# Kernel optimization log

Measured on AMD Instinct MI355X. Metric: run time of the kernel, lower is better.

The kernel has to match this reference:

```python
import jax, jax.numpy as jnp
import numpy as np
from jax import lax

# Dims: c1=256, num_heads = c1//64 = 4, head_dim=64, key_dim=32 (attn_ratio=0.5)
B, C, H, W = 4, 256, 64, 64
NH, HD, KD = 4, 64, 32
HQKV = C + 2 * NH * KD  # 512
RED = 16  # channel-attention reduction


def setup_inputs() -> dict:
    key = jax.random.key(0)
    ks = jax.random.split(key, 11)
    s = 0.02
    return {
        "x": jax.random.normal(ks[0], (B, C, H, W), jnp.float32),
        # Attention params (Conv = conv+BN folded into conv+bias)
        "w_qkv": jax.random.normal(ks[1], (HQKV, C), jnp.float32) * s,   # 1x1 conv
        "b_qkv": jax.random.normal(ks[2], (HQKV,), jnp.float32) * s,
        "w_proj": jax.random.normal(ks[3], (C, C), jnp.float32) * s,     # 1x1 conv
        "b_proj": jax.random.normal(ks[4], (C,), jnp.float32) * s,
        "w_pe": jax.random.normal(ks[5], (C, 1, 3, 3), jnp.float32) * s, # depthwise 3x3
        "b_pe": jax.random.normal(ks[6], (C,), jnp.float32) * s,
        # ChannelAttention params (1x1 convs, no bias)
        "w_fc1": jax.random.normal(ks[7], (C // RED, C), jnp.float32) * s,
        "w_fc2": jax.random.normal(ks[8], (C, C // RED), jnp.float32) * s,
        # SpatialAttention conv (2->1 channels, 3x3, no bias)
        "w_sa": jax.random.normal(ks[9], (1, 2, 3, 3), jnp.float32) * s,
    }


def _conv1x1(x, w, b=None):
    y = jnp.einsum('bchw,oc->bohw', x, w)
    if b is not None:
        y = y + b[None, :, None, None]
    return y


def _dwconv3(x, w, b):
    y = lax.conv_general_dilated(
        x, w, window_strides=(1, 1), padding='SAME',
        feature_group_count=x.shape[1],
        dimension_numbers=('NCHW', 'OIHW', 'NCHW'))
    return y + b[None, :, None, None]


def reference(x, w_qkv, b_qkv, w_proj, b_proj, w_pe, b_pe, w_fc1, w_fc2, w_sa):
    Bb, Cc, Hh, Ww = x.shape
    N = Hh * Ww
    scale = KD ** -0.5

    # --- Attention (asymmetric q/k/v head dims) ---
    qkv = _conv1x1(x, w_qkv, b_qkv).reshape(Bb, NH, 2 * KD + HD, N)
    q = qkv[:, :, :KD]            # [B,h,KD,N]
    k = qkv[:, :, KD:2 * KD]      # [B,h,KD,N]
    v = qkv[:, :, 2 * KD:]        # [B,h,HD,N]
    attn = jnp.einsum('bhkn,bhkm->bhnm', q, k) * scale  # [B,h,N,N]
    attn = jax.nn.softmax(attn, axis=-1)
    out = jnp.einsum('bhdm,bhnm->bhdn', v, attn).reshape(Bb, Cc, Hh, Ww)
    out = out + _dwconv3(v.reshape(Bb, Cc, Hh, Ww), w_pe, b_pe)
    out = _conv1x1(out, w_proj, b_proj)
    x = x + out

    # --- Channel attention (shared MLP on avg+max pooled features) ---
    def mlp(u):  # u: [B,C]
        return jnp.maximum(u @ w_fc1.T, 0.0) @ w_fc2.T
    avg = jnp.mean(x, axis=(2, 3))
    mx = jnp.max(x, axis=(2, 3))
    ca = jax.nn.sigmoid(mlp(avg) + mlp(mx))[:, :, None, None]
    x = x * ca

    # --- Spatial attention ---
    sa_in = jnp.stack([jnp.mean(x, axis=1), jnp.max(x, axis=1)], axis=1)  # [B,2,H,W]
    sa = lax.conv_general_dilated(
        sa_in, w_sa, window_strides=(1, 1), padding='SAME',
        dimension_numbers=('NCHW', 'OIHW', 'NCHW'))
    sa = jax.nn.sigmoid(sa)
    return x * sa
```

## Files before the change

### kernel.cpp

```cpp
#include <hip/hip_runtime.h>
#include <hip/hip_bf16.h>

typedef __bf16 bf16;
typedef __bf16 bf16x4 __attribute__((ext_vector_type(4)));
typedef __bf16 bf16x8 __attribute__((ext_vector_type(8)));
typedef float f32x4 __attribute__((ext_vector_type(4)));

#define B_ 4
#define C_ 256
#define NH_ 4
#define KD_ 32
#define HD_ 64
#define N_ 4096
#define HQKV_ 512

__global__ __launch_bounds__(256) void k_convw(const float* wq, const float* wp,
                                               bf16* wqb, bf16* wpb) {
    int i = blockIdx.x * 256 + threadIdx.x;
    if (i < HQKV_ * C_) wqb[i] = (bf16)wq[i];
    if (i < C_ * C_)    wpb[i] = (bf16)wp[i];
}

__global__ __launch_bounds__(256) void k_transpose(const float* __restrict__ x,
                                                   bf16* __restrict__ xT) {
    __shared__ float tile[64][65];
    int b = blockIdx.z, c0 = blockIdx.y * 64, n0 = blockIdx.x * 64;
    int t = threadIdx.x;
    int lane = t & 63, wv = t >> 6;
    for (int k = 0; k < 16; ++k) {
        int cl = k * 4 + wv;
        tile[cl][lane] = x[((size_t)(b * C_ + c0 + cl)) * N_ + n0 + lane];
    }
    __syncthreads();
    for (int k = 0; k < 16; ++k) {
        int nl = k * 4 + wv;
        xT[((size_t)(b * N_ + n0 + nl)) * C_ + c0 + lane] = (bf16)tile[lane][nl];
    }
}

__global__ __launch_bounds__(256) void k_qkv(const bf16* __restrict__ wqb,
                                             const bf16* __restrict__ xT,
                                             const float* __restrict__ bias,
                                             bf16* __restrict__ qt, bf16* __restrict__ kt,
                                             bf16* __restrict__ vb) {
    int n0 = blockIdx.x * 64, o0 = blockIdx.y * 64, b = blockIdx.z;
    int t = threadIdx.x, w = t >> 6, l = t & 63, lr = l & 15, lg = l >> 4;
    const bf16* arow = wqb + (size_t)(o0 + 16 * w + lr) * C_ + 8 * lg;
    const bf16* brow = xT + ((size_t)b * N_ + n0 + lr) * C_ + 8 * lg;
    f32x4 acc[4];
    f32x4 zz = {0.f, 0.f, 0.f, 0.f};
    acc[0] = zz; acc[1] = zz; acc[2] = zz; acc[3] = zz;
    for (int kk = 0; kk < C_; kk += 32) {
        bf16x8 a = *(const bf16x8*)(arow + kk);
#pragma unroll
        for (int tt = 0; tt < 4; ++tt) {
            bf16x8 bb = *(const bf16x8*)(brow + (size_t)tt * 16 * C_ + kk);
            acc[tt] = __builtin_amdgcn_mfma_f32_16x16x32_bf16(a, bb, acc[tt], 0, 0, 0);
        }
    }
    const float scale = 0.25506953076085663f;
#pragma unroll
    for (int tt = 0; tt < 4; ++tt) {
        int n = n0 + 16 * tt + lr;
#pragma unroll
        for (int j = 0; j < 4; ++j) {
            int o = o0 + 16 * w + 4 * lg + j;
            float val = acc[tt][j] + bias[o];
            int h = o >> 7, r = o & 127;
            size_t bh = (size_t)(b * NH_ + h);
            if (r < KD_)            qt[(bh * N_ + n) * KD_ + r] = (bf16)(val * scale);
            else if (r < 2 * KD_)   kt[(bh * N_ + n) * KD_ + (r - KD_)] = (bf16)val;
            else                    vb[(bh * HD_ + (r - 2 * KD_)) * N_ + n] = (bf16)val;
        }
    }
}

__global__ __launch_bounds__(256) void k_attn(const bf16* __restrict__ qt,
                                              const bf16* __restrict__ kt,
                                              const bf16* __restrict__ vb,
                                              float* __restrict__ attnT) {
    __shared__ bf16 ldsK[2][64 * KD_];
    __shared__ bf16 ldsV[2][64 * 64];
    __shared__ bf16 ldsP[4][32 * 72];
    int n0 = blockIdx.x * 128;
    int bh = blockIdx.y;
    int b = bh >> 2, h = bh & 3;
    int t = threadIdx.x, w = t >> 6, l = t & 63, lr = l & 15, lg = l >> 4;

    bf16x8 aq0 = *(const bf16x8*)(qt + ((size_t)bh * N_ + n0 + 32 * w + lr) * KD_ + 8 * lg);
    bf16x8 aq1 = *(const bf16x8*)(qt + ((size_t)bh * N_ + n0 + 32 * w + 16 + lr) * KD_ + 8 * lg);

    int krow = 16 * w + (l >> 2);
    const bf16* kg = kt + ((size_t)bh * N_ + krow) * KD_ + 8 * (l & 3);
    bf16* kwp = &ldsK[0][0] + krow * KD_ + 8 * ((l & 3) ^ (krow & 3));
    int vrow0 = 16 * w + (l >> 3);
    int vrow1 = vrow0 + 8;
    const bf16* vg0 = vb + ((size_t)bh * HD_ + vrow0) * N_ + 8 * (l & 7);
    const bf16* vg1 = vb + ((size_t)bh * HD_ + vrow1) * N_ + 8 * (l & 7);
    bf16* vwp0 = &ldsV[0][0] + vrow0 * 64 + 8 * ((l & 7) ^ (vrow0 & 7));
    bf16* vwp1 = &ldsV[0][0] + vrow1 * 64 + 8 * ((l & 7) ^ (vrow1 & 7));

    f32x4 zz = {0.f, 0.f, 0.f, 0.f};
    f32x4 Lacc0 = zz, Lacc1 = zz;
    f32x4 oacc[2][4];
#pragma unroll
    for (int q = 0; q < 2; ++q)
#pragma unroll
        for (int dt = 0; dt < 4; ++dt) oacc[q][dt] = zz;
    bf16* myp = &ldsP[w][0];

    bf16x8 rk = *(const bf16x8*)(kg);
    bf16x8 rv0 = *(const bf16x8*)(vg0);
    bf16x8 rv1 = *(const bf16x8*)(vg1);

    int cur = 0;
    for (int m0 = 0; m0 < N_; m0 += 64) {
        *(bf16x8*)(kwp + cur * (64 * KD_)) = rk;
        *(bf16x8*)(vwp0 + cur * (64 * 64)) = rv0;
        *(bf16x8*)(vwp1 + cur * (64 * 64)) = rv1;
        if (m0 + 64 < N_) {
            rk  = *(const bf16x8*)(kg + (size_t)(m0 + 64) * KD_);
            rv0 = *(const bf16x8*)(vg0 + m0 + 64);
            rv1 = *(const bf16x8*)(vg1 + m0 + 64);
        }
        __syncthreads();
        const bf16* kb_ = &ldsK[cur][0];
        const bf16* vb_ = &ldsV[cur][0];
        f32x4 s0[4], s1[4];
#pragma unroll
        for (int tt = 0; tt < 4; ++tt) {
            bf16x8 kf = *(const bf16x8*)(kb_ + (16 * tt + lr) * KD_ + 8 * (lg ^ (lr & 3)));
            s0[tt] = __builtin_amdgcn_mfma_f32_16x16x32_bf16(kf, aq0, zz, 0, 0, 0);
            s1[tt] = __builtin_amdgcn_mfma_f32_16x16x32_bf16(kf, aq1, zz, 0, 0, 0);
        }
#pragma unroll
        for (int tt = 0; tt < 4; ++tt) {
            bf16x4 p0, p1;
#pragma unroll
            for (int j = 0; j < 4; ++j) {
                float pv0 = __builtin_amdgcn_exp2f(s0[tt][j]);
                float pv1 = __builtin_amdgcn_exp2f(s1[tt][j]);
                Lacc0[j] += pv0; Lacc1[j] += pv1;
                p0[j] = (bf16)pv0; p1[j] = (bf16)pv1;
            }
            *(bf16x4*)(myp + lr * 72 + 16 * tt + 4 * lg) = p0;
            *(bf16x4*)(myp + (16 + lr) * 72 + 16 * tt + 4 * lg) = p1;
        }
#pragma unroll
        for (int ks = 0; ks < 2; ++ks) {
            bf16x8 pa0 = *(const bf16x8*)(myp + lr * 72 + 32 * ks + 8 * lg);
            bf16x8 pa1 = *(const bf16x8*)(myp + (16 + lr) * 72 + 32 * ks + 8 * lg);
#pragma unroll
            for (int dt = 0; dt < 4; ++dt) {
                bf16x8 vf = *(const bf16x8*)(vb_ + (16 * dt + lr) * 64 + 8 * ((4 * ks + lg) ^ (lr & 7)));
                oacc[0][dt] = __builtin_amdgcn_mfma_f32_16x16x32_bf16(pa0, vf, oacc[0][dt], 0, 0, 0);
                oacc[1][dt] = __builtin_amdgcn_mfma_f32_16x16x32_bf16(pa1, vf, oacc[1][dt], 0, 0, 0);
            }
        }
        cur ^= 1;
    }
    float Lp0 = Lacc0[0] + Lacc0[1] + Lacc0[2] + Lacc0[3];
    float Lp1 = Lacc1[0] + Lacc1[1] + Lacc1[2] + Lacc1[3];
    Lp0 += __shfl_xor(Lp0, 16); Lp0 += __shfl_xor(Lp0, 32);
    Lp1 += __shfl_xor(Lp1, 16); Lp1 += __shfl_xor(Lp1, 32);
    float inv0[4], inv1[4];
#pragma unroll
    for (int j = 0; j < 4; ++j) {
        inv0[j] = 1.f / __shfl(Lp0, 4 * lg + j);
        inv1[j] = 1.f / __shfl(Lp1, 4 * lg + j);
    }
#pragma unroll
    for (int dt = 0; dt < 4; ++dt)
#pragma unroll
        for (int j = 0; j < 4; ++j) {
            int n = n0 + 32 * w + 4 * lg + j;
            int d = h * HD_ + 16 * dt + lr;
            attnT[((size_t)b * N_ + n) * C_ + d] = oacc[0][dt][j] * inv0[j];
            attnT[((size_t)b * N_ + n + 16) * C_ + d] = oacc[1][dt][j] * inv1[j];
        }
}

__global__ __launch_bounds__(256) void k_pe_add(const float* __restrict__ attnT,
                                                const bf16* __restrict__ vb,
                                                const float* __restrict__ wpe,
                                                const float* __restrict__ bpe,
                                                bf16* __restrict__ yT) {
    __shared__ float vt[64 * 199];
    int hh = blockIdx.x, c0 = blockIdx.y * 64, b = blockIdx.z;
    int t = threadIdx.x, lane = t & 63, wg = t >> 6;

    if (t < 192) {
        int c_l = t >> 2, kh2 = t & 3;
        if (kh2 < 3) {
            vt[c_l * 199 + kh2 * 66 + 0] = 0.f;
            vt[c_l * 199 + kh2 * 66 + 65] = 0.f;
        }
    }
    if (t >= 192) {
        int u = t - 192;
        int c_l = 48 + (u >> 2), kh2 = u & 3;
        if (kh2 < 3) {
            vt[c_l * 199 + kh2 * 66 + 0] = 0.f;
            vt[c_l * 199 + kh2 * 66 + 65] = 0.f;
        }
    }
#pragma unroll
    for (int kh = 0; kh < 3; ++kh) {
        int hh2 = hh + kh - 1;
        bool ok = (hh2 >= 0 && hh2 < 64);
        for (int ci = 0; ci < 16; ++ci) {
            int c_l = wg * 16 + ci;
            float val = ok ? (float)vb[((size_t)(b * C_ + c0 + c_l)) * N_ + hh2 * 64 + lane] : 0.f;
            vt[c_l * 199 + kh * 66 + 1 + lane] = val;
        }
    }
    __syncthreads();

    int c = c0 + lane;
    float w9[9];
#pragma unroll
    for (int k = 0; k < 9; ++k) w9[k] = wpe[c * 9 + k];
    float bc = bpe[c];
    const float* vrow = vt + lane * 199;

#pragma unroll
    for (int wi = 0; wi < 16; ++wi) {
        int w = wg * 16 + wi;
        float acc = bc;
#pragma unroll
        for (int kh = 0; kh < 3; ++kh)
#pragma unroll
            for (int kw = 0; kw < 3; ++kw)
                acc += vrow[kh * 66 + w + kw] * w9[kh * 3 + kw];
        int n = hh * 64 + w;
        size_t idx = ((size_t)b * N_ + n) * C_ + c;
        yT[idx] = (bf16)(attnT[idx] + acc);
    }
}

__global__ __launch_bounds__(256) void k_proj(const bf16* __restrict__ wpb,
                                              const bf16* __restrict__ yT,
                                              const float* __restrict__ bias,
                                              const float* __restrict__ x,
                                              float* __restrict__ x2) {
    int n0 = blockIdx.x * 64, o0 = blockIdx.y * 64, b = blockIdx.z;
    int t = threadIdx.x, w = t >> 6, l = t & 63, lr = l & 15, lg = l >> 4;
    const bf16* arow = wpb + (size_t)(o0 + 16 * w + lr) * C_ + 8 * lg;
    const bf16* brow = yT + ((size_t)b * N_ + n0 + lr) * C_ + 8 * lg;
    f32x4 acc[4];
    f32x4 zz = {0.f, 0.f, 0.f, 0.f};
    acc[0] = zz; acc[1] = zz; acc[2] = zz; acc[3] = zz;
    for (int kk = 0; kk < C_; kk += 32) {
        bf16x8 a = *(const bf16x8*)(arow + kk);
#pragma unroll
        for (int tt = 0; tt < 4; ++tt) {
            bf16x8 bb = *(const bf16x8*)(brow + (size_t)tt * 16 * C_ + kk);
            acc[tt] = __builtin_amdgcn_mfma_f32_16x16x32_bf16(a, bb, acc[tt], 0, 0, 0);
        }
    }
#pragma unroll
    for (int tt = 0; tt < 4; ++tt) {
        int n = n0 + 16 * tt + lr;
#pragma unroll
        for (int j = 0; j < 4; ++j) {
            int o = o0 + 16 * w + 4 * lg + j;
            size_t idx = ((size_t)b * C_ + o) * N_ + n;
            x2[idx] = x[idx] + acc[tt][j] + bias[o];
        }
    }
}

__global__ __launch_bounds__(256) void k_ca_red(const float* __restrict__ x2,
                                                float* __restrict__ avg, float* __restrict__ mx) {
    int bc = blockIdx.x;
    int t = threadIdx.x;
    const float* row = x2 + (size_t)bc * N_;
    float s = 0.f, m = -1e30f;
    for (int i = t; i < N_; i += 256) { float v = row[i]; s += v; m = fmaxf(m, v); }
#pragma unroll
    for (int d = 1; d < 64; d <<= 1) { s += __shfl_xor(s, d); m = fmaxf(m, __shfl_xor(m, d)); }
    __shared__ float ss[4], sm[4];
    int w = t >> 6;
    if ((t & 63) == 0) { ss[w] = s; sm[w] = m; }
    __syncthreads();
    if (t == 0) {
        avg[bc] = (ss[0] + ss[1] + ss[2] + ss[3]) / (float)N_;
        mx[bc] = fmaxf(fmaxf(sm[0], sm[1]), fmaxf(sm[2], sm[3]));
    }
}

__global__ __launch_bounds__(256) void k_ca_mlp(const float* __restrict__ avg,
                                                const float* __restrict__ mx,
                                                const float* __restrict__ wfc1,
                                                const float* __restrict__ wfc2,
                                                float* __restrict__ ca) {
    int b = blockIdx.x, t = threadIdx.x;
    __shared__ float hsum[16];
    if (t < 16) {
        const float* w1 = wfc1 + t * C_;
        float ha = 0.f, hm = 0.f;
        for (int c = 0; c < C_; ++c) { ha += avg[b * C_ + c] * w1[c]; hm += mx[b * C_ + c] * w1[c]; }
        hsum[t] = fmaxf(ha, 0.f) + fmaxf(hm, 0.f);
    }
    __syncthreads();
    float o = 0.f;
    const float* w2 = wfc2 + t * 16;
#pragma unroll
    for (int r = 0; r < 16; ++r) o += hsum[r] * w2[r];
    ca[b * C_ + t] = 1.f / (1.f + __expf(-o));
}

__global__ __launch_bounds__(256) void k_sa_red(const float* __restrict__ x2,
                                                const float* __restrict__ ca,
                                                float* __restrict__ sain) {
    int b = blockIdx.y;
    int n = blockIdx.x * 256 + threadIdx.x;
    __shared__ float cal[C_];
    cal[threadIdx.x] = ca[b * C_ + threadIdx.x];
    __syncthreads();
    float s = 0.f, m = -1e30f;
    for (int c = 0; c < C_; ++c) {
        float v = x2[((size_t)b * C_ + c) * N_ + n] * cal[c];
        s += v; m = fmaxf(m, v);
    }
    sain[((size_t)b * 2 + 0) * N_ + n] = s * (1.f / C_);
    sain[((size_t)b * 2 + 1) * N_ + n] = m;
}

__global__ __launch_bounds__(256) void k_final(const float* __restrict__ x2,
                                               const float* __restrict__ ca,
                                               const float* __restrict__ sain,
                                               const float* __restrict__ wsa,
                                               float* __restrict__ out) {
    int b = blockIdx.y;
    int n = blockIdx.x * 256 + threadIdx.x;
    __shared__ float cal[C_];
    cal[threadIdx.x] = ca[b * C_ + threadIdx.x];
    __syncthreads();
    int hh = n >> 6, ww = n & 63;
    float acc = 0.f;
#pragma unroll
    for (int i = 0; i < 2; ++i)
#pragma unroll
        for (int kh = 0; kh < 3; ++kh) {
            int hh2 = hh + kh - 1;
            if (hh2 < 0 || hh2 >= 64) continue;
#pragma unroll
            for (int kw = 0; kw < 3; ++kw) {
                int ww2 = ww + kw - 1;
                if (ww2 < 0 || ww2 >= 64) continue;
                acc += sain[((size_t)b * 2 + i) * N_ + hh2 * 64 + ww2] * wsa[i * 9 + kh * 3 + kw];
            }
        }
    float sa = 1.f / (1.f + __expf(-acc));
    for (int c = 0; c < C_; ++c) {
        size_t idx = ((size_t)b * C_ + c) * N_ + n;
        out[idx] = x2[idx] * cal[c] * sa;
    }
}

extern "C" void kernel_launch(void* const* d_in, const int* in_sizes, int n_in,
                              void* d_out, int out_size, void* d_ws, size_t ws_size,
                              hipStream_t stream) {
    const float* x     = (const float*)d_in[0];
    const float* wqkv  = (const float*)d_in[1];
    const float* bqkv  = (const float*)d_in[2];
    const float* wproj = (const float*)d_in[3];
    const float* bproj = (const float*)d_in[4];
    const float* wpe   = (const float*)d_in[5];
    const float* bpe   = (const float*)d_in[6];
    const float* wfc1  = (const float*)d_in[7];
    const float* wfc2  = (const float*)d_in[8];
    const float* wsa   = (const float*)d_in[9];
    float* out = (float*)d_out;

    char* ws = (char*)d_ws;
    size_t off = 0;
    auto alloc = [&](size_t bytes) {
        char* p = ws + off;
        off += (bytes + 255) & ~(size_t)255;
        return p;
    };
    bf16*  qt    = (bf16*)alloc((size_t)B_ * NH_ * N_ * KD_ * 2);
    bf16*  ktb   = (bf16*)alloc((size_t)B_ * NH_ * N_ * KD_ * 2);
    bf16*  vbuf  = (bf16*)alloc((size_t)B_ * NH_ * HD_ * N_ * 2);
    bf16*  xT    = (bf16*)alloc((size_t)B_ * N_ * C_ * 2);
    float* attnT = (float*)alloc((size_t)B_ * N_ * C_ * 4);
    float* x2    = (float*)alloc((size_t)B_ * C_ * N_ * 4);
    bf16*  wqb   = (bf16*)alloc((size_t)HQKV_ * C_ * 2);
    bf16*  wpb   = (bf16*)alloc((size_t)C_ * C_ * 2);
    float* avg   = (float*)alloc(B_ * C_ * 4);
    float* mxb   = (float*)alloc(B_ * C_ * 4);
    float* cab   = (float*)alloc(B_ * C_ * 4);
    float* sain  = (float*)alloc((size_t)B_ * 2 * N_ * 4);
    bf16*  yT    = xT;

    k_convw<<<dim3((HQKV_ * C_ + 255) / 256), 256, 0, stream>>>(wqkv, wproj, wqb, wpb);
    k_transpose<<<dim3(64, 4, B_), 256, 0, stream>>>(x, xT);
    k_qkv<<<dim3(64, 8, B_), 256, 0, stream>>>(wqb, xT, bqkv, qt, ktb, vbuf);
    k_attn<<<dim3(32, B_ * NH_), 256, 0, stream>>>(qt, ktb, vbuf, attnT);
    k_pe_add<<<dim3(64, 4, B_), 256, 0, stream>>>(attnT, vbuf, wpe, bpe, yT);
    k_proj<<<dim3(64, 4, B_), 256, 0, stream>>>(wpb, yT, bproj, x, x2);
    k_ca_red<<<dim3(B_ * C_), 256, 0, stream>>>(x2, avg, mxb);
    k_ca_mlp<<<dim3(B_), 256, 0, stream>>>(avg, mxb, wfc1, wfc2, cab);
    k_sa_red<<<dim3(16, B_), 256, 0, stream>>>(x2, cab, sain);
    k_final<<<dim3(16, B_), 256, 0, stream>>>(x2, cab, sain, wsa, out);
}
```

Baseline: 233.9 us.

## Process two key tiles per barrier in attention, interleave exp with MFMA, store bf16

New measurement: 227.6 us. 1.03x faster.

```diff
diff --git a/kernel.cpp b/kernel.cpp
--- a/kernel.cpp
+++ b/kernel.cpp
@@ -78,12 +78,13 @@
 __global__ __launch_bounds__(256) void k_attn(const bf16* __restrict__ qt,
                                               const bf16* __restrict__ kt,
                                               const bf16* __restrict__ vb,
-                                              float* __restrict__ attnT) {
-    __shared__ bf16 ldsK[2][64 * KD_];
-    __shared__ bf16 ldsV[2][64 * 64];
+                                              bf16* __restrict__ attnT) {
+    __shared__ bf16 ldsK[2][2][64 * KD_];
+    __shared__ bf16 ldsV[2][2][64 * 64];
     __shared__ bf16 ldsP[4][32 * 72];
-    int n0 = blockIdx.x * 128;
-    int bh = blockIdx.y;
+    int id = blockIdx.x;
+    int bh = id & 15;
+    int n0 = (id >> 4) * 128;
     int b = bh >> 2, h = bh & 3;
     int t = threadIdx.x, w = t >> 6, l = t & 63, lr = l & 15, lg = l >> 4;
 
@@ -92,13 +93,12 @@
 
     int krow = 16 * w + (l >> 2);
     const bf16* kg = kt + ((size_t)bh * N_ + krow) * KD_ + 8 * (l & 3);
-    bf16* kwp = &ldsK[0][0] + krow * KD_ + 8 * ((l & 3) ^ (krow & 3));
-    int vrow0 = 16 * w + (l >> 3);
-    int vrow1 = vrow0 + 8;
+    int kwo = krow * KD_ + 8 * ((l & 3) ^ (krow & 3));
+    int vrow0 = 16 * w + (l >> 3), vrow1 = vrow0 + 8;
     const bf16* vg0 = vb + ((size_t)bh * HD_ + vrow0) * N_ + 8 * (l & 7);
     const bf16* vg1 = vb + ((size_t)bh * HD_ + vrow1) * N_ + 8 * (l & 7);
-    bf16* vwp0 = &ldsV[0][0] + vrow0 * 64 + 8 * ((l & 7) ^ (vrow0 & 7));
-    bf16* vwp1 = &ldsV[0][0] + vrow1 * 64 + 8 * ((l & 7) ^ (vrow1 & 7));
+    int vwo0 = vrow0 * 64 + 8 * ((l & 7) ^ (vrow0 & 7));
+    int vwo1 = vrow1 * 64 + 8 * ((l & 7) ^ (vrow1 & 7));
 
     f32x4 zz = {0.f, 0.f, 0.f, 0.f};
     f32x4 Lacc0 = zz, Lacc1 = zz;
@@ -109,43 +109,90 @@
         for (int dt = 0; dt < 4; ++dt) oacc[q][dt] = zz;
     bf16* myp = &ldsP[w][0];
 
-    bf16x8 rk = *(const bf16x8*)(kg);
-    bf16x8 rv0 = *(const bf16x8*)(vg0);
-    bf16x8 rv1 = *(const bf16x8*)(vg1);
-
-    int cur = 0;
-    for (int m0 = 0; m0 < N_; m0 += 64) {
-        *(bf16x8*)(kwp + cur * (64 * KD_)) = rk;
-        *(bf16x8*)(vwp0 + cur * (64 * 64)) = rv0;
-        *(bf16x8*)(vwp1 + cur * (64 * 64)) = rv1;
-        if (m0 + 64 < N_) {
-            rk  = *(const bf16x8*)(kg + (size_t)(m0 + 64) * KD_);
-            rv0 = *(const bf16x8*)(vg0 + m0 + 64);
-            rv1 = *(const bf16x8*)(vg1 + m0 + 64);
+    bf16x8 rka  = *(const bf16x8*)(kg);
+    bf16x8 rkb  = *(const bf16x8*)(kg + (size_t)64 * KD_);
+    bf16x8 rva0 = *(const bf16x8*)(vg0);
+    bf16x8 rva1 = *(const bf16x8*)(vg1);
+    bf16x8 rvb0 = *(const bf16x8*)(vg0 + 64);
+    bf16x8 rvb1 = *(const bf16x8*)(vg1 + 64);
+
+    int p = 0;
+    for (int m0 = 0; m0 < N_; m0 += 128, p ^= 1) {
+        *(bf16x8*)(&ldsK[p][0][0] + kwo)  = rka;
+        *(bf16x8*)(&ldsK[p][1][0] + kwo)  = rkb;
+        *(bf16x8*)(&ldsV[p][0][0] + vwo0) = rva0;
+        *(bf16x8*)(&ldsV[p][0][0] + vwo1) = rva1;
+        *(bf16x8*)(&ldsV[p][1][0] + vwo0) = rvb0;
+        *(bf16x8*)(&ldsV[p][1][0] + vwo1) = rvb1;
+        if (m0 + 128 < N_) {
+            rka  = *(const bf16x8*)(kg + (size_t)(m0 + 128) * KD_);
+            rkb  = *(const bf16x8*)(kg + (size_t)(m0 + 192) * KD_);
+            rva0 = *(const bf16x8*)(vg0 + m0 + 128);
+            rva1 = *(const bf16x8*)(vg1 + m0 + 128);
+            rvb0 = *(const bf16x8*)(vg0 + m0 + 192);
+            rvb1 = *(const bf16x8*)(vg1 + m0 + 192);
         }
         __syncthreads();
-        const bf16* kb_ = &ldsK[cur][0];
-        const bf16* vb_ = &ldsV[cur][0];
-        f32x4 s0[4], s1[4];
+        const bf16* ka_ = &ldsK[p][0][0];
+        const bf16* kb_ = &ldsK[p][1][0];
+        const bf16* va_ = &ldsV[p][0][0];
+        const bf16* vb_ = &ldsV[p][1][0];
+
+        f32x4 sa0[4], sa1[4], sb0[4], sb1[4];
+        __builtin_amdgcn_s_setprio(1);
+#pragma unroll
+        for (int tt = 0; tt < 4; ++tt) {
+            bf16x8 kf = *(const bf16x8*)(ka_ + (16 * tt + lr) * KD_ + 8 * (lg ^ (lr & 3)));
+            sa0[tt] = __builtin_amdgcn_mfma_f32_16x16x32_bf16(kf, aq0, zz, 0, 0, 0);
+            sa1[tt] = __builtin_amdgcn_mfma_f32_16x16x32_bf16(kf, aq1, zz, 0, 0, 0);
+        }
 #pragma unroll
         for (int tt = 0; tt < 4; ++tt) {
             bf16x8 kf = *(const bf16x8*)(kb_ + (16 * tt + lr) * KD_ + 8 * (lg ^ (lr & 3)));
-            s0[tt] = __builtin_amdgcn_mfma_f32_16x16x32_bf16(kf, aq0, zz, 0, 0, 0);
-            s1[tt] = __builtin_amdgcn_mfma_f32_16x16x32_bf16(kf, aq1, zz, 0, 0, 0);
-        }
+            sb0[tt] = __builtin_amdgcn_mfma_f32_16x16x32_bf16(kf, aq0, zz, 0, 0, 0);
+            sb1[tt] = __builtin_amdgcn_mfma_f32_16x16x32_bf16(kf, aq1, zz, 0, 0, 0);
+        }
+        __builtin_amdgcn_s_setprio(0);
 #pragma unroll
         for (int tt = 0; tt < 4; ++tt) {
             bf16x4 p0, p1;
 #pragma unroll
             for (int j = 0; j < 4; ++j) {
-                float pv0 = __builtin_amdgcn_exp2f(s0[tt][j]);
-                float pv1 = __builtin_amdgcn_exp2f(s1[tt][j]);
+                float pv0 = __builtin_amdgcn_exp2f(sa0[tt][j]);
+                float pv1 = __builtin_amdgcn_exp2f(sa1[tt][j]);
                 Lacc0[j] += pv0; Lacc1[j] += pv1;
                 p0[j] = (bf16)pv0; p1[j] = (bf16)pv1;
             }
             *(bf16x4*)(myp + lr * 72 + 16 * tt + 4 * lg) = p0;
             *(bf16x4*)(myp + (16 + lr) * 72 + 16 * tt + 4 * lg) = p1;
         }
+        __builtin_amdgcn_s_setprio(1);
+#pragma unroll
+        for (int ks = 0; ks < 2; ++ks) {
+            bf16x8 pa0 = *(const bf16x8*)(myp + lr * 72 + 32 * ks + 8 * lg);
+            bf16x8 pa1 = *(const bf16x8*)(myp + (16 + lr) * 72 + 32 * ks + 8 * lg);
+#pragma unroll
+            for (int dt = 0; dt < 4; ++dt) {
+                bf16x8 vf = *(const bf16x8*)(va_ + (16 * dt + lr) * 64 + 8 * ((4 * ks + lg) ^ (lr & 7)));
+                oacc[0][dt] = __builtin_amdgcn_mfma_f32_16x16x32_bf16(pa0, vf, oacc[0][dt], 0, 0, 0);
+                oacc[1][dt] = __builtin_amdgcn_mfma_f32_16x16x32_bf16(pa1, vf, oacc[1][dt], 0, 0, 0);
+            }
+        }
+        __builtin_amdgcn_s_setprio(0);
+#pragma unroll
+        for (int tt = 0; tt < 4; ++tt) {
+            bf16x4 p0, p1;
+#pragma unroll
+            for (int j = 0; j < 4; ++j) {
+                float pv0 = __builtin_amdgcn_exp2f(sb0[tt][j]);
+                float pv1 = __builtin_amdgcn_exp2f(sb1[tt][j]);
+                Lacc0[j] += pv0; Lacc1[j] += pv1;
+                p0[j] = (bf16)pv0; p1[j] = (bf16)pv1;
+            }
+            *(bf16x4*)(myp + lr * 72 + 16 * tt + 4 * lg) = p0;
+            *(bf16x4*)(myp + (16 + lr) * 72 + 16 * tt + 4 * lg) = p1;
+        }
+        __builtin_amdgcn_s_setprio(1);
 #pragma unroll
         for (int ks = 0; ks < 2; ++ks) {
             bf16x8 pa0 = *(const bf16x8*)(myp + lr * 72 + 32 * ks + 8 * lg);
@@ -157,7 +204,7 @@
                 oacc[1][dt] = __builtin_amdgcn_mfma_f32_16x16x32_bf16(pa1, vf, oacc[1][dt], 0, 0, 0);
             }
         }
-        cur ^= 1;
+        __builtin_amdgcn_s_setprio(0);
     }
     float Lp0 = Lacc0[0] + Lacc0[1] + Lacc0[2] + Lacc0[3];
     float Lp1 = Lacc1[0] + Lacc1[1] + Lacc1[2] + Lacc1[3];
@@ -175,12 +222,12 @@
         for (int j = 0; j < 4; ++j) {
             int n = n0 + 32 * w + 4 * lg + j;
             int d = h * HD_ + 16 * dt + lr;
-            attnT[((size_t)b * N_ + n) * C_ + d] = oacc[0][dt][j] * inv0[j];
-            attnT[((size_t)b * N_ + n + 16) * C_ + d] = oacc[1][dt][j] * inv1[j];
-        }
-}
-
-__global__ __launch_bounds__(256) void k_pe_add(const float* __restrict__ attnT,
+            attnT[((size_t)b * N_ + n) * C_ + d] = (bf16)(oacc[0][dt][j] * inv0[j]);
+            attnT[((size_t)b * N_ + n + 16) * C_ + d] = (bf16)(oacc[1][dt][j] * inv1[j]);
+        }
+}
+
+__global__ __launch_bounds__(256) void k_pe_add(const bf16* __restrict__ attnT,
                                                 const bf16* __restrict__ vb,
                                                 const float* __restrict__ wpe,
                                                 const float* __restrict__ bpe,
@@ -234,7 +281,7 @@
                 acc += vrow[kh * 66 + w + kw] * w9[kh * 3 + kw];
         int n = hh * 64 + w;
         size_t idx = ((size_t)b * N_ + n) * C_ + c;
-        yT[idx] = (bf16)(attnT[idx] + acc);
+        yT[idx] = (bf16)((float)attnT[idx] + acc);
     }
 }
 
@@ -385,7 +432,7 @@
     bf16*  ktb   = (bf16*)alloc((size_t)B_ * NH_ * N_ * KD_ * 2);
     bf16*  vbuf  = (bf16*)alloc((size_t)B_ * NH_ * HD_ * N_ * 2);
     bf16*  xT    = (bf16*)alloc((size_t)B_ * N_ * C_ * 2);
-    float* attnT = (float*)alloc((size_t)B_ * N_ * C_ * 4);
+    bf16*  attnT = (bf16*)alloc((size_t)B_ * N_ * C_ * 2);
     float* x2    = (float*)alloc((size_t)B_ * C_ * N_ * 4);
     bf16*  wqb   = (bf16*)alloc((size_t)HQKV_ * C_ * 2);
     bf16*  wpb   = (bf16*)alloc((size_t)C_ * C_ * 2);
@@ -398,7 +445,7 @@
     k_convw<<<dim3((HQKV_ * C_ + 255) / 256), 256, 0, stream>>>(wqkv, wproj, wqb, wpb);
     k_transpose<<<dim3(64, 4, B_), 256, 0, stream>>>(x, xT);
     k_qkv<<<dim3(64, 8, B_), 256, 0, stream>>>(wqb, xT, bqkv, qt, ktb, vbuf);
-    k_attn<<<dim3(32, B_ * NH_), 256, 0, stream>>>(qt, ktb, vbuf, attnT);
+    k_attn<<<dim3(512), 256, 0, stream>>>(qt, ktb, vbuf, attnT);
     k_pe_add<<<dim3(64, 4, B_), 256, 0, stream>>>(attnT, vbuf, wpe, bpe, yT);
     k_proj<<<dim3(64, 4, B_), 256, 0, stream>>>(wpb, yT, bproj, x, x2);
     k_ca_red<<<dim3(B_ * C_), 256, 0, stream>>>(x2, avg, mxb);
```

## Shrink attention query tile to 64 rows, swizzle P buffer, store output as bf16

Applied to the files above, without the earlier changes.

Result: faster. 228.6 us (-2.3%).

```diff
diff --git a/kernel.cpp b/kernel.cpp
--- a/kernel.cpp
+++ b/kernel.cpp
@@ -75,112 +75,100 @@
     }
 }
 
-__global__ __launch_bounds__(256) void k_attn(const bf16* __restrict__ qt,
-                                              const bf16* __restrict__ kt,
-                                              const bf16* __restrict__ vb,
-                                              float* __restrict__ attnT) {
+__global__ __launch_bounds__(256, 4) void k_attn(const bf16* __restrict__ qt,
+                                                 const bf16* __restrict__ kt,
+                                                 const bf16* __restrict__ vb,
+                                                 bf16* __restrict__ attnT) {
     __shared__ bf16 ldsK[2][64 * KD_];
     __shared__ bf16 ldsV[2][64 * 64];
-    __shared__ bf16 ldsP[4][32 * 72];
-    int n0 = blockIdx.x * 128;
-    int bh = blockIdx.y;
+    __shared__ bf16 ldsP[4][16 * 64];
+    int id = blockIdx.x;
+    int bh = id & 15;
+    int n0 = (id >> 4) * 64;
     int b = bh >> 2, h = bh & 3;
     int t = threadIdx.x, w = t >> 6, l = t & 63, lr = l & 15, lg = l >> 4;
 
-    bf16x8 aq0 = *(const bf16x8*)(qt + ((size_t)bh * N_ + n0 + 32 * w + lr) * KD_ + 8 * lg);
-    bf16x8 aq1 = *(const bf16x8*)(qt + ((size_t)bh * N_ + n0 + 32 * w + 16 + lr) * KD_ + 8 * lg);
+    bf16x8 aq = *(const bf16x8*)(qt + ((size_t)bh * N_ + n0 + 16 * w + lr) * KD_ + 8 * lg);
 
     int krow = 16 * w + (l >> 2);
     const bf16* kg = kt + ((size_t)bh * N_ + krow) * KD_ + 8 * (l & 3);
-    bf16* kwp = &ldsK[0][0] + krow * KD_ + 8 * ((l & 3) ^ (krow & 3));
-    int vrow0 = 16 * w + (l >> 3);
-    int vrow1 = vrow0 + 8;
-    const bf16* vg0 = vb + ((size_t)bh * HD_ + vrow0) * N_ + 8 * (l & 7);
-    const bf16* vg1 = vb + ((size_t)bh * HD_ + vrow1) * N_ + 8 * (l & 7);
-    bf16* vwp0 = &ldsV[0][0] + vrow0 * 64 + 8 * ((l & 7) ^ (vrow0 & 7));
-    bf16* vwp1 = &ldsV[0][0] + vrow1 * 64 + 8 * ((l & 7) ^ (vrow1 & 7));
+    int kwo = krow * KD_ + 8 * ((l & 3) ^ (krow & 3));
+    int vrow = 16 * w + (l >> 3);
+    const bf16* vg = vb + ((size_t)bh * HD_ + vrow) * N_ + 8 * (l & 7);
+    int vwo = vrow * 64 + 8 * ((l & 7) ^ (vrow & 7));
 
     f32x4 zz = {0.f, 0.f, 0.f, 0.f};
-    f32x4 Lacc0 = zz, Lacc1 = zz;
-    f32x4 oacc[2][4];
-#pragma unroll
-    for (int q = 0; q < 2; ++q)
-#pragma unroll
-        for (int dt = 0; dt < 4; ++dt) oacc[q][dt] = zz;
-    bf16* myp = &ldsP[w][0];
-
-    bf16x8 rk = *(const bf16x8*)(kg);
-    bf16x8 rv0 = *(const bf16x8*)(vg0);
-    bf16x8 rv1 = *(const bf16x8*)(vg1);
+    f32x4 Lacc = zz;
+    f32x4 oacc[4];
+    oacc[0] = zz; oacc[1] = zz; oacc[2] = zz; oacc[3] = zz;
+    char* myp = (char*)&ldsP[w][0];
+
+    bf16x8 rk  = *(const bf16x8*)(kg);
+    bf16x8 rv0 = *(const bf16x8*)(vg);
+    bf16x8 rv1 = *(const bf16x8*)(vg + (size_t)8 * N_);
 
     int cur = 0;
-    for (int m0 = 0; m0 < N_; m0 += 64) {
-        *(bf16x8*)(kwp + cur * (64 * KD_)) = rk;
-        *(bf16x8*)(vwp0 + cur * (64 * 64)) = rv0;
-        *(bf16x8*)(vwp1 + cur * (64 * 64)) = rv1;
+    for (int m0 = 0; m0 < N_; m0 += 64, cur ^= 1) {
+        *(bf16x8*)(&ldsK[cur][0] + kwo) = rk;
+        *(bf16x8*)(&ldsV[cur][0] + vwo) = rv0;
+        *(bf16x8*)(&ldsV[cur][0] + vwo + 8 * 64) = rv1;
         if (m0 + 64 < N_) {
             rk  = *(const bf16x8*)(kg + (size_t)(m0 + 64) * KD_);
-            rv0 = *(const bf16x8*)(vg0 + m0 + 64);
-            rv1 = *(const bf16x8*)(vg1 + m0 + 64);
+            rv0 = *(const bf16x8*)(vg + m0 + 64);
+            rv1 = *(const bf16x8*)(vg + (size_t)8 * N_ + m0 + 64);
         }
         __syncthreads();
         const bf16* kb_ = &ldsK[cur][0];
         const bf16* vb_ = &ldsV[cur][0];
-        f32x4 s0[4], s1[4];
+
+        f32x4 s[4];
+        __builtin_amdgcn_s_setprio(1);
 #pragma unroll
         for (int tt = 0; tt < 4; ++tt) {
             bf16x8 kf = *(const bf16x8*)(kb_ + (16 * tt + lr) * KD_ + 8 * (lg ^ (lr & 3)));
-            s0[tt] = __builtin_amdgcn_mfma_f32_16x16x32_bf16(kf, aq0, zz, 0, 0, 0);
-            s1[tt] = __builtin_amdgcn_mfma_f32_16x16x32_bf16(kf, aq1, zz, 0, 0, 0);
-        }
+            s[tt] = __builtin_amdgcn_mfma_f32_16x16x32_bf16(kf, aq, zz, 0, 0, 0);
+        }
+        __builtin_amdgcn_s_setprio(0);
 #pragma unroll
         for (int tt = 0; tt < 4; ++tt) {
-            bf16x4 p0, p1;
-#pragma unroll
-            for (int j = 0; j < 4; ++j) {
-                float pv0 = __builtin_amdgcn_exp2f(s0[tt][j]);
-                float pv1 = __builtin_amdgcn_exp2f(s1[tt][j]);
-                Lacc0[j] += pv0; Lacc1[j] += pv1;
-                p0[j] = (bf16)pv0; p1[j] = (bf16)pv1;
-            }
-            *(bf16x4*)(myp + lr * 72 + 16 * tt + 4 * lg) = p0;
-            *(bf16x4*)(myp + (16 + lr) * 72 + 16 * tt + 4 * lg) = p1;
-        }
+            f32x4 pv;
+#pragma unroll
+            for (int j = 0; j < 4; ++j) pv[j] = __builtin_amdgcn_exp2f(s[tt][j]);
+            Lacc += pv;
+            bf16x4 pk;
+#pragma unroll
+            for (int j = 0; j < 4; ++j) pk[j] = (bf16)pv[j];
+            *(bf16x4*)(myp + lr * 128 + (((2 * tt + (lg >> 1)) ^ (lr & 7)) << 4) + 8 * (lg & 1)) = pk;
+        }
+        __builtin_amdgcn_s_setprio(1);
 #pragma unroll
         for (int ks = 0; ks < 2; ++ks) {
-            bf16x8 pa0 = *(const bf16x8*)(myp + lr * 72 + 32 * ks + 8 * lg);
-            bf16x8 pa1 = *(const bf16x8*)(myp + (16 + lr) * 72 + 32 * ks + 8 * lg);
+            bf16x8 pa = *(const bf16x8*)(myp + lr * 128 + (((4 * ks + lg) ^ (lr & 7)) << 4));
 #pragma unroll
             for (int dt = 0; dt < 4; ++dt) {
                 bf16x8 vf = *(const bf16x8*)(vb_ + (16 * dt + lr) * 64 + 8 * ((4 * ks + lg) ^ (lr & 7)));
-                oacc[0][dt] = __builtin_amdgcn_mfma_f32_16x16x32_bf16(pa0, vf, oacc[0][dt], 0, 0, 0);
-                oacc[1][dt] = __builtin_amdgcn_mfma_f32_16x16x32_bf16(pa1, vf, oacc[1][dt], 0, 0, 0);
+                oacc[dt] = __builtin_amdgcn_mfma_f32_16x16x32_bf16(pa, vf, oacc[dt], 0, 0, 0);
             }
         }
-        cur ^= 1;
-    }
-    float Lp0 = Lacc0[0] + Lacc0[1] + Lacc0[2] + Lacc0[3];
-    float Lp1 = Lacc1[0] + Lacc1[1] + Lacc1[2] + Lacc1[3];
-    Lp0 += __shfl_xor(Lp0, 16); Lp0 += __shfl_xor(Lp0, 32);
-    Lp1 += __shfl_xor(Lp1, 16); Lp1 += __shfl_xor(Lp1, 32);
-    float inv0[4], inv1[4];
-#pragma unroll
-    for (int j = 0; j < 4; ++j) {
-        inv0[j] = 1.f / __shfl(Lp0, 4 * lg + j);
-        inv1[j] = 1.f / __shfl(Lp1, 4 * lg + j);
-    }
+        __builtin_amdgcn_s_setprio(0);
+    }
+    float Lp = Lacc[0] + Lacc[1] + Lacc[2] + Lacc[3];
+    Lp += __shfl_xor(Lp, 16);
+    Lp += __shfl_xor(Lp, 32);
+    float inv[4];
+#pragma unroll
+    for (int j = 0; j < 4; ++j) inv[j] = 1.f / __shfl(Lp, 4 * lg + j);
 #pragma unroll
     for (int dt = 0; dt < 4; ++dt)
 #pragma unroll
         for (int j = 0; j < 4; ++j) {
-            int n = n0 + 32 * w + 4 * lg + j;
+            int n = n0 + 16 * w + 4 * lg + j;
             int d = h * HD_ + 16 * dt + lr;
-            attnT[((size_t)b * N_ + n) * C_ + d] = oacc[0][dt][j] * inv0[j];
-            attnT[((size_t)b * N_ + n + 16) * C_ + d] = oacc[1][dt][j] * inv1[j];
-        }
-}
-
-__global__ __launch_bounds__(256) void k_pe_add(const float* __restrict__ attnT,
+            attnT[((size_t)b * N_ + n) * C_ + d] = (bf16)(oacc[dt][j] * inv[j]);
+        }
+}
+
+__global__ __launch_bounds__(256) void k_pe_add(const bf16* __restrict__ attnT,
                                                 const bf16* __restrict__ vb,
                                                 const float* __restrict__ wpe,
                                                 const float* __restrict__ bpe,
@@ -234,7 +222,7 @@
                 acc += vrow[kh * 66 + w + kw] * w9[kh * 3 + kw];
         int n = hh * 64 + w;
         size_t idx = ((size_t)b * N_ + n) * C_ + c;
-        yT[idx] = (bf16)(attnT[idx] + acc);
+        yT[idx] = (bf16)((float)attnT[idx] + acc);
     }
 }
 
@@ -385,7 +373,7 @@
     bf16*  ktb   = (bf16*)alloc((size_t)B_ * NH_ * N_ * KD_ * 2);
     bf16*  vbuf  = (bf16*)alloc((size_t)B_ * NH_ * HD_ * N_ * 2);
     bf16*  xT    = (bf16*)alloc((size_t)B_ * N_ * C_ * 2);
-    float* attnT = (float*)alloc((size_t)B_ * N_ * C_ * 4);
+    bf16*  attnT = (bf16*)alloc((size_t)B_ * N_ * C_ * 2);
     float* x2    = (float*)alloc((size_t)B_ * C_ * N_ * 4);
     bf16*  wqb   = (bf16*)alloc((size_t)HQKV_ * C_ * 2);
     bf16*  wpb   = (bf16*)alloc((size_t)C_ * C_ * 2);
@@ -398,7 +386,7 @@
     k_convw<<<dim3((HQKV_ * C_ + 255) / 256), 256, 0, stream>>>(wqkv, wproj, wqb, wpb);
     k_transpose<<<dim3(64, 4, B_), 256, 0, stream>>>(x, xT);
     k_qkv<<<dim3(64, 8, B_), 256, 0, stream>>>(wqb, xT, bqkv, qt, ktb, vbuf);
-    k_attn<<<dim3(32, B_ * NH_), 256, 0, stream>>>(qt, ktb, vbuf, attnT);
+    k_attn<<<dim3(1024), 256, 0, stream>>>(qt, ktb, vbuf, attnT);
     k_pe_add<<<dim3(64, 4, B_), 256, 0, stream>>>(attnT, vbuf, wpe, bpe, yT);
     k_proj<<<dim3(64, 4, B_), 256, 0, stream>>>(wpb, yT, bproj, x, x2);
     k_ca_red<<<dim3(B_ * C_), 256, 0, stream>>>(x2, avg, mxb);
```
